# Performance work log

Measured on AMD Instinct MI355X. Metric: run time of the kernel, lower is better.

The kernel has to match this reference:

```python
import jax, jax.numpy as jnp
import numpy as np

B, S, D, H = 4, 1024, 1024, 16
DH = D // H  # 64
SCALE = 1.0 / np.sqrt(D)  # module uses 1/sqrt(d_model), not d_head


def _mh(t):
    # [B,S,D] -> [B*H,S,DH]
    b, s, _ = t.shape
    return t.reshape(b, s, H, DH).transpose(0, 2, 1, 3).reshape(b * H, s, DH)


def _shift(t):
    # pad one zero at FRONT of last dim, reinterpret (row-major) as [BH,L+1,S], drop first row
    bh, s, l = t.shape
    t = jnp.concatenate([jnp.zeros((bh, s, 1), t.dtype), t], axis=-1)
    return t.reshape(bh, l + 1, s)[:, 1:, :]


def setup_inputs() -> dict:
    key = jax.random.key(0)
    ks = jax.random.split(key, 12)
    w_sc = 1.0 / np.sqrt(D)
    return {
        "x": jax.random.normal(ks[0], (B, S, D), jnp.float32),
        "u": jax.random.normal(ks[1], (DH,), jnp.float32) * 0.02,
        "v": jax.random.normal(ks[2], (DH,), jnp.float32) * 0.02,
        "pos": jax.random.normal(ks[3], (B, S, D), jnp.float32),
        "Wq": jax.random.normal(ks[4], (D, D), jnp.float32) * w_sc,
        "bq": jnp.zeros((D,), jnp.float32),
        "Wk": jax.random.normal(ks[5], (D, D), jnp.float32) * w_sc,
        "bk": jnp.zeros((D,), jnp.float32),
        "Wv": jax.random.normal(ks[6], (D, D), jnp.float32) * w_sc,
        "bv": jnp.zeros((D,), jnp.float32),
        "Wc": jax.random.normal(ks[7], (D, D), jnp.float32) * w_sc,
        "bc": jnp.zeros((D,), jnp.float32),
    }


def reference(x, u, v, pos, Wq, bq, Wk, bk, Wv, bv, Wc, bc):
    q = _mh(x @ Wq.T + bq)      # [BH,S,DH]
    k = _mh(x @ Wk.T + bk)      # [BH,S,DH]
    w = _mh(x @ Wv.T + bv)      # [BH,S,DH]
    r = _mh(pos)                # [BH,S,DH]
    ac = jnp.einsum('bjk,bmk->bjm', q + u, k)          # content-content  [BH,S,S]
    bd = _shift(jnp.einsum('bjk,blk->bjl', q + v, r))  # content-position [BH,S,S]
    att = jax.nn.softmax((ac + bd) * SCALE, axis=-1)   # dropout is identity (eval)
    o = att @ w                                        # [BH,S,DH]
    o = o.reshape(B, H, S, DH).transpose(0, 2, 1, 3).reshape(B, S, D)
    return o @ Wc.T + bc
```

## Files before the change

kernel.cpp:

```cpp
#include <hip/hip_runtime.h>
#include <hip/hip_bf16.h>


typedef __bf16 bf16x8 __attribute__((ext_vector_type(8)));
typedef float  f32x4  __attribute__((ext_vector_type(4)));
typedef unsigned short u16x4 __attribute__((ext_vector_type(4)));

struct alignas(16) U128 { unsigned long long lo, hi; };

__device__ __forceinline__ bf16x8 ldg8(const __hip_bfloat16* p) {
    U128 u = *reinterpret_cast<const U128*>(p);
    return __builtin_bit_cast(bf16x8, u);
}

__device__ __forceinline__ __bf16 f2b(float f) {
    __hip_bfloat16 h = __float2bfloat16(f);
    return __builtin_bit_cast(__bf16, h);
}
__device__ __forceinline__ unsigned short f2bu(float f) {
    __hip_bfloat16 h = __float2bfloat16(f);
    return __builtin_bit_cast(unsigned short, h);
}
__device__ __forceinline__ float b2f(__bf16 b) {
    __hip_bfloat16 h = __builtin_bit_cast(__hip_bfloat16, b);
    return __bfloat162float(h);
}

__device__ __forceinline__ bf16x8 ldg8cvt(const float* p) {
    f32x4 a = *reinterpret_cast<const f32x4*>(p);
    f32x4 b = *reinterpret_cast<const f32x4*>(p + 4);
    bf16x8 r;
    r[0] = f2b(a[0]); r[1] = f2b(a[1]); r[2] = f2b(a[2]); r[3] = f2b(a[3]);
    r[4] = f2b(b[0]); r[5] = f2b(b[1]); r[6] = f2b(b[2]); r[7] = f2b(b[3]);
    return r;
}

#define MFMA16(a, b, c) __builtin_amdgcn_mfma_f32_16x16x32_bf16((a), (b), (c), 0, 0, 0)

__device__ __forceinline__ void gll16(const __hip_bfloat16* g, void* lds_wave_base) {
    __builtin_amdgcn_global_load_lds(
        (const __attribute__((address_space(1))) void*)g,
        (__attribute__((address_space(3))) void*)lds_wave_base,
        16, 0, 0);
}

__global__ __launch_bounds__(256) void cvt_kernel(
    const float* __restrict__ x,  const float* __restrict__ pos,
    const float* __restrict__ wq, const float* __restrict__ wk,
    const float* __restrict__ wv, const float* __restrict__ wc,
    __hip_bfloat16* __restrict__ xb, __hip_bfloat16* __restrict__ posb,
    __hip_bfloat16* __restrict__ wqkvb, __hip_bfloat16* __restrict__ wcb)
{
    const size_t base = ((size_t)blockIdx.x * 256 + threadIdx.x) * 8;
    const size_t M1 = (size_t)1 << 20;
    const float* src; __hip_bfloat16* dst; size_t o;
    if (base < 4*M1)        { src = x;   dst = xb;           o = base; }
    else if (base < 8*M1)   { src = pos; dst = posb;         o = base - 4*M1; }
    else if (base < 9*M1)   { src = wq;  dst = wqkvb;        o = base - 8*M1; }
    else if (base < 10*M1)  { src = wk;  dst = wqkvb + M1;   o = base - 9*M1; }
    else if (base < 11*M1)  { src = wv;  dst = wqkvb + 2*M1; o = base - 10*M1; }
    else                    { src = wc;  dst = wcb;          o = base - 11*M1; }
    *(bf16x8*)(dst + o) = ldg8cvt(src + o);
}

__global__ __launch_bounds__(256) void gemm_qkv(
    const __hip_bfloat16* __restrict__ A,
    const __hip_bfloat16* __restrict__ Bm,
    const float* __restrict__ bq, const float* __restrict__ bk,
    const float* __restrict__ bv, const float* __restrict__ u,
    __hip_bfloat16* __restrict__ Qu,
    __hip_bfloat16* __restrict__ Kb, __hip_bfloat16* __restrict__ Vt)
{
    __shared__ __hip_bfloat16 As[128 * 32];
    __shared__ __hip_bfloat16 Bs[128 * 32];

    const int tid  = threadIdx.x;
    const int lane = tid & 63, w = tid >> 6;
    const int quad = lane >> 4, c16 = lane & 15;
    const int wm = w >> 1, wn = w & 1;
    const int m0 = blockIdx.y * 128;
    const int n0 = blockIdx.x * 128;

    const int srow = w * 16 + (lane >> 2);
    const int scol = (lane & 3) * 8;
    const __hip_bfloat16* gA0 = A  + (size_t)(m0 + srow) * 1024 + scol;
    const __hip_bfloat16* gA1 = gA0 + (size_t)64 * 1024;
    const __hip_bfloat16* gB0 = Bm + (size_t)(n0 + srow) * 1024 + scol;
    const __hip_bfloat16* gB1 = gB0 + (size_t)64 * 1024;
    char* ldsA0 = (char*)As + (w << 10);
    char* ldsA1 = ldsA0 + 4096;
    char* ldsB0 = (char*)Bs + (w << 10);
    char* ldsB1 = ldsB0 + 4096;

    f32x4 acc[4][4] = {};

    for (int k0 = 0; k0 < 1024; k0 += 32) {
        gll16(gA0 + k0, ldsA0);
        gll16(gA1 + k0, ldsA1);
        gll16(gB0 + k0, ldsB0);
        gll16(gB1 + k0, ldsB1);
        __syncthreads();

        bf16x8 af[4], bfr[4];
        #pragma unroll
        for (int i = 0; i < 4; ++i) {
            af[i]  = *(const bf16x8*)&As[(wm * 64 + i * 16 + c16) * 32 + quad * 8];
            bfr[i] = *(const bf16x8*)&Bs[(wn * 64 + i * 16 + c16) * 32 + quad * 8];
        }
        #pragma unroll
        for (int mi = 0; mi < 4; ++mi)
            #pragma unroll
            for (int ni = 0; ni < 4; ++ni)
                acc[mi][ni] = MFMA16(af[mi], bfr[ni], acc[mi][ni]);
        __syncthreads();
    }

    #pragma unroll
    for (int mi = 0; mi < 4; ++mi) {
        #pragma unroll
        for (int ni = 0; ni < 4; ++ni) {
            const int m = m0 + wm * 64 + mi * 16 + quad * 4;
            const int n = n0 + wn * 64 + ni * 16 + c16;
            if (n < 1024) {
                const float b0 = bq[n] + u[n & 63];
                #pragma unroll
                for (int r = 0; r < 4; ++r)
                    Qu[(size_t)(m + r) * 1024 + n] =
                        __float2bfloat16(acc[mi][ni][r] + b0);
            } else if (n < 2048) {
                const int nn = n - 1024;
                const float b0 = bk[nn];
                #pragma unroll
                for (int r = 0; r < 4; ++r)
                    Kb[(size_t)(m + r) * 1024 + nn] =
                        __float2bfloat16(acc[mi][ni][r] + b0);
            } else {
                const int nn = n - 2048;
                const float b0 = bv[nn];
                const int d = nn & 63, hh = nn >> 6;
                const int bb = m >> 10, s = m & 1023;
                u16x4 pk;
                #pragma unroll
                for (int r = 0; r < 4; ++r)
                    pk[r] = f2bu(acc[mi][ni][r] + b0);
                *(u16x4*)&Vt[(((size_t)(bb * 16 + hh) * 64 + d) << 10) + s] = pk;
            }
        }
    }
}

__global__ __launch_bounds__(256) void gemm_fin64(
    const __hip_bfloat16* __restrict__ A,
    const __hip_bfloat16* __restrict__ Bm,
    float* __restrict__ dout, const float* __restrict__ bc)
{
    __shared__ __hip_bfloat16 As[64 * 32];
    __shared__ __hip_bfloat16 Bs[64 * 32];

    const int tid  = threadIdx.x;
    const int lane = tid & 63, w = tid >> 6;
    const int quad = lane >> 4, c16 = lane & 15;
    const int wm = w >> 1, wn = w & 1;
    const int m0 = blockIdx.y * 64;
    const int n0 = blockIdx.x * 64;

    const int srow = w * 16 + (lane >> 2);
    const int scol = (lane & 3) * 8;
    const __hip_bfloat16* gA = A  + (size_t)(m0 + srow) * 1024 + scol;
    const __hip_bfloat16* gB = Bm + (size_t)(n0 + srow) * 1024 + scol;
    char* ldsA = (char*)As + (w << 10);
    char* ldsB = (char*)Bs + (w << 10);

    f32x4 acc[2][2] = {};

    for (int k0 = 0; k0 < 1024; k0 += 32) {
        gll16(gA + k0, ldsA);
        gll16(gB + k0, ldsB);
        __syncthreads();

        bf16x8 af[2], bfr[2];
        #pragma unroll
        for (int i = 0; i < 2; ++i) {
            af[i]  = *(const bf16x8*)&As[(wm * 32 + i * 16 + c16) * 32 + quad * 8];
            bfr[i] = *(const bf16x8*)&Bs[(wn * 32 + i * 16 + c16) * 32 + quad * 8];
        }
        #pragma unroll
        for (int mi = 0; mi < 2; ++mi)
            #pragma unroll
            for (int ni = 0; ni < 2; ++ni)
                acc[mi][ni] = MFMA16(af[mi], bfr[ni], acc[mi][ni]);
        __syncthreads();
    }

    #pragma unroll
    for (int mi = 0; mi < 2; ++mi) {
        #pragma unroll
        for (int ni = 0; ni < 2; ++ni) {
            const int m = m0 + wm * 32 + mi * 16 + quad * 4;
            const int n = n0 + wn * 32 + ni * 16 + c16;
            const float b0 = bc[n];
            #pragma unroll
            for (int r = 0; r < 4; ++r)
                dout[(size_t)(m + r) * 1024 + n] = acc[mi][ni][r] + b0;
        }
    }
}

__device__ __forceinline__ int lidx16(int row, int c) {
    return (row << 10) + ((((c >> 3) ^ row) << 3) | (c & 7));
}

__global__ __launch_bounds__(512) void attn_kernel(
    const __hip_bfloat16* __restrict__ Qu,
    const __hip_bfloat16* __restrict__ Kb,
    const __hip_bfloat16* __restrict__ Posb,
    const __hip_bfloat16* __restrict__ Vt,
    const float* __restrict__ uvec, const float* __restrict__ vvec,
    __hip_bfloat16* __restrict__ O)
{
    __shared__ __hip_bfloat16 Ls[64 * 1024];
    __shared__ float q2s[64];
    __shared__ float Wsum[64 * 8];
    __shared__ float rs[64];

    const int tid  = threadIdx.x;
    const int lane = tid & 63, w = tid >> 6;
    const int quad = lane >> 4, c16 = lane & 15;
    const int i0 = blockIdx.y * 64;
    const int bh = blockIdx.x;
    const int b = bh >> 4, h = bh & 15;
    const size_t headoff = (size_t)h * 64;
    const size_t tokbase = (size_t)b * 1024;
    const int j2 = i0 + 64;

    if (tid < 64) {
        float val = 0.f;
        if (j2 < 1024)
            val = b2f(__builtin_bit_cast(__bf16,
                      Qu[(tokbase + j2) * 1024 + headoff + tid])) +
                  (vvec[tid] - uvec[tid]);
        q2s[tid] = val;
    }
    __syncthreads();

    if (tid < 64) {
        const int i = i0 + tid;
        if (i + 1 < 1024) Ls[lidx16(tid, i + 1)] = __float2bfloat16(0.f);
    }

    const __hip_bfloat16* qup0 =
        Qu + (tokbase + i0 + c16) * 1024 + headoff + quad * 8;

    {
        bf16x8 a[4][2];
        #pragma unroll
        for (int g = 0; g < 4; ++g) {
            a[g][0] = ldg8(qup0 + (size_t)g * 16 * 1024);
            a[g][1] = ldg8(qup0 + (size_t)g * 16 * 1024 + 32);
            #pragma unroll
            for (int j = 0; j < 8; ++j) {
                const int d = quad * 8 + j;
                a[g][0][j] = f2b(b2f(a[g][0][j]) + (vvec[d] - uvec[d]));
                a[g][1][j] = f2b(b2f(a[g][1][j]) + (vvec[d + 32] - uvec[d + 32]));
            }
        }
        for (int t = 0; t < 8; ++t) {
            const int l0 = w * 128 + t * 16;
            const __hip_bfloat16* rp =
                Posb + (tokbase + l0 + c16) * 1024 + headoff + quad * 8;
            const bf16x8 r0 = ldg8(rp);
            const bf16x8 r1 = ldg8(rp + 32);
            const int l = l0 + c16;
            #pragma unroll
            for (int g = 0; g < 4; ++g) {
                f32x4 c = (f32x4){0.f, 0.f, 0.f, 0.f};
                c = MFMA16(a[g][0], r0, c);
                c = MFMA16(a[g][1], r1, c);
                #pragma unroll
                for (int r = 0; r < 4; ++r) {
                    const int jl = g * 16 + quad * 4 + r;
                    const int j  = i0 + jl;
                    const __bf16 val = f2b(c[r]);
                    if (l >= 1023 - j) Ls[lidx16(jl, l + j - 1023)] =
                        __builtin_bit_cast(__hip_bfloat16, val);
                    if (jl >= 1 && l <= 1022 - j) Ls[lidx16(jl - 1, l + j + 1)] =
                        __builtin_bit_cast(__hip_bfloat16, val);
                }
            }
        }
    }

    if (j2 < 1024) {
        for (int c = i0 + 65 + tid; c < 1024; c += 512) {
            const int l = c - i0 - 65;
            const __hip_bfloat16* rp = Posb + (tokbase + l) * 1024 + headoff;
            float s = 0.f;
            #pragma unroll
            for (int d8 = 0; d8 < 8; ++d8) {
                const bf16x8 rv = ldg8(rp + d8 * 8);
                #pragma unroll
                for (int j = 0; j < 8; ++j)
                    s += q2s[d8 * 8 + j] * b2f(rv[j]);
            }
            Ls[lidx16(63, c)] = __float2bfloat16(s);
        }
    }
    __syncthreads();

    {
        bf16x8 au[4][2];
        #pragma unroll
        for (int g = 0; g < 4; ++g) {
            au[g][0] = ldg8(qup0 + (size_t)g * 16 * 1024);
            au[g][1] = ldg8(qup0 + (size_t)g * 16 * 1024 + 32);
        }
        const float C1 = 1.44269504f * 0.03125f;
        const float C2 = -5.77078016f;
        float sums[4][4] = {};
        for (int t = 0; t < 8; ++t) {
            const int c0 = w * 128 + t * 16;
            const __hip_bfloat16* kp =
                Kb + (tokbase + c0 + c16) * 1024 + headoff + quad * 8;
            const bf16x8 k0 = ldg8(kp);
            const bf16x8 k1 = ldg8(kp + 32);
            const int cc = c0 + c16;
            #pragma unroll
            for (int g = 0; g < 4; ++g) {
                f32x4 c = (f32x4){0.f, 0.f, 0.f, 0.f};
                c = MFMA16(au[g][0], k0, c);
                c = MFMA16(au[g][1], k1, c);
                #pragma unroll
                for (int r = 0; r < 4; ++r) {
                    const int il = g * 16 + quad * 4 + r;
                    const int idx = lidx16(il, cc);
                    const float lg = __bfloat162float(Ls[idx]) + c[r];
                    const float p = __builtin_amdgcn_exp2f(fmaf(lg, C1, C2));
                    sums[g][r] += p;
                    Ls[idx] = __float2bfloat16(p);
                }
            }
        }
        #pragma unroll
        for (int g = 0; g < 4; ++g)
            #pragma unroll
            for (int r = 0; r < 4; ++r) {
                float s = sums[g][r];
                s += __shfl_xor(s, 1);
                s += __shfl_xor(s, 2);
                s += __shfl_xor(s, 4);
                s += __shfl_xor(s, 8);
                if (c16 == 0) Wsum[(g * 16 + quad * 4 + r) * 8 + w] = s;
            }
    }
    __syncthreads();

    if (tid < 64) {
        float s = 0.f;
        #pragma unroll
        for (int k = 0; k < 8; ++k) s += Wsum[tid * 8 + k];
        rs[tid] = 1.f / s;
    }
    __syncthreads();

    {
        const int d0 = (w & 3) * 16;
        const int kh = w >> 2;
        const __hip_bfloat16* vp =
            Vt + ((size_t)bh * 64 + d0 + c16) * 1024 + quad * 8;
        f32x4 acc[4] = {};
        for (int kk = kh * 512; kk < kh * 512 + 512; kk += 32) {
            const bf16x8 vld = ldg8(vp + kk);
            #pragma unroll
            for (int g = 0; g < 4; ++g) {
                const bf16x8 p =
                    *(const bf16x8*)&Ls[lidx16(g * 16 + c16, kk + quad * 8)];
                acc[g] = MFMA16(p, vld, acc[g]);
            }
        }
        __syncthreads();
        float* Lf = (float*)Ls;
        const int sbase = (w & 3) * 1024;
        if (kh == 1) {
            #pragma unroll
            for (int g = 0; g < 4; ++g)
                #pragma unroll
                for (int r = 0; r < 4; ++r)
                    Lf[sbase + g * 256 + (quad * 4 + r) * 16 + c16] = acc[g][r];
        }
        __syncthreads();
        if (kh == 0) {
            #pragma unroll
            for (int g = 0; g < 4; ++g)
                #pragma unroll
                for (int r = 0; r < 4; ++r) {
                    const int il = g * 16 + quad * 4 + r;
                    const float val =
                        (acc[g][r] + Lf[sbase + g * 256 + (quad * 4 + r) * 16 + c16])
                        * rs[il];
                    const int i = i0 + il;
                    const int d = d0 + c16;
                    O[(tokbase + i) * 1024 + headoff + d] = __float2bfloat16(val);
                }
        }
    }
}

extern "C" void kernel_launch(void* const* d_in, const int* in_sizes, int n_in,
                              void* d_out, int out_size, void* d_ws, size_t ws_size,
                              hipStream_t stream)
{
    const float* x   = (const float*)d_in[0];
    const float* u   = (const float*)d_in[1];
    const float* v   = (const float*)d_in[2];
    const float* pos = (const float*)d_in[3];
    const float* Wq  = (const float*)d_in[4];
    const float* bq  = (const float*)d_in[5];
    const float* Wk  = (const float*)d_in[6];
    const float* bk  = (const float*)d_in[7];
    const float* Wv  = (const float*)d_in[8];
    const float* bv  = (const float*)d_in[9];
    const float* Wc  = (const float*)d_in[10];
    const float* bc  = (const float*)d_in[11];

    const size_t MB = (size_t)1 << 20;
    char* ws = (char*)d_ws;
    __hip_bfloat16* Qu    = (__hip_bfloat16*)(ws + 0 * MB);
    __hip_bfloat16* Kb    = (__hip_bfloat16*)(ws + 8 * MB);
    __hip_bfloat16* Vt    = (__hip_bfloat16*)(ws + 16 * MB);
    __hip_bfloat16* xb    = (__hip_bfloat16*)(ws + 24 * MB);
    __hip_bfloat16* O     = (__hip_bfloat16*)(ws + 24 * MB);
    __hip_bfloat16* Posb  = (__hip_bfloat16*)(ws + 32 * MB);
    __hip_bfloat16* Wqkvb = (__hip_bfloat16*)(ws + 40 * MB);
    __hip_bfloat16* Wcb   = (__hip_bfloat16*)(ws + 46 * MB);

    cvt_kernel<<<6144, 256, 0, stream>>>(x, pos, Wq, Wk, Wv, Wc,
                                         xb, Posb, Wqkvb, Wcb);

    gemm_qkv<<<dim3(24, 32), dim3(256), 0, stream>>>(
        xb, Wqkvb, bq, bk, bv, u, Qu, Kb, Vt);

    attn_kernel<<<dim3(64, 16), dim3(512), 0, stream>>>(
        Qu, Kb, Posb, Vt, u, v, O);

    gemm_fin64<<<dim3(16, 64), dim3(256), 0, stream>>>(
        O, Wcb, (float*)d_out, bc);
}
```

Measured before the change: 281.9 us.

## Halve attention query tile to 32 rows and transpose MFMA operands for vectorized LDS access

Each attention block now handles 32 query rows instead of 64. That halves the 128KB LDS score buffer to 64KB and doubles the grid, with launch bounds hinting more resident blocks per CU. The MFMA operands are swapped so each lane holds four consecutive columns of one row. This allows packed 4-element LDS reads and writes of scores and probabilities, a simpler shift index computation, and fewer cross-lane reductions. The cost is that K, V and positional data are reloaded from global memory twice as often per query row.

```diff
diff --git a/kernel.cpp b/kernel.cpp
--- a/kernel.cpp
+++ b/kernel.cpp
@@ -23,6 +23,10 @@
 }
 __device__ __forceinline__ float b2f(__bf16 b) {
     __hip_bfloat16 h = __builtin_bit_cast(__hip_bfloat16, b);
+    return __bfloat162float(h);
+}
+__device__ __forceinline__ float bu2f(unsigned short u) {
+    __hip_bfloat16 h = __builtin_bit_cast(__hip_bfloat16, u);
     return __bfloat162float(h);
 }
 
@@ -210,7 +214,7 @@
     return (row << 10) + ((((c >> 3) ^ row) << 3) | (c & 7));
 }
 
-__global__ __launch_bounds__(512) void attn_kernel(
+__global__ __launch_bounds__(512, 4) void attn_kernel(
     const __hip_bfloat16* __restrict__ Qu,
     const __hip_bfloat16* __restrict__ Kb,
     const __hip_bfloat16* __restrict__ Posb,
@@ -218,20 +222,20 @@
     const float* __restrict__ uvec, const float* __restrict__ vvec,
     __hip_bfloat16* __restrict__ O)
 {
-    __shared__ __hip_bfloat16 Ls[64 * 1024];
+    __shared__ __attribute__((aligned(16))) __hip_bfloat16 Ls[32 * 1024];
     __shared__ float q2s[64];
-    __shared__ float Wsum[64 * 8];
-    __shared__ float rs[64];
+    __shared__ float Wsum[32 * 8];
+    __shared__ float rs[32];
 
     const int tid  = threadIdx.x;
     const int lane = tid & 63, w = tid >> 6;
     const int quad = lane >> 4, c16 = lane & 15;
-    const int i0 = blockIdx.y * 64;
+    const int i0 = blockIdx.y * 32;
     const int bh = blockIdx.x;
     const int b = bh >> 4, h = bh & 15;
     const size_t headoff = (size_t)h * 64;
     const size_t tokbase = (size_t)b * 1024;
-    const int j2 = i0 + 64;
+    const int j2 = i0 + 32;
 
     if (tid < 64) {
         float val = 0.f;
@@ -243,7 +247,7 @@
     }
     __syncthreads();
 
-    if (tid < 64) {
+    if (tid < 32) {
         const int i = i0 + tid;
         if (i + 1 < 1024) Ls[lidx16(tid, i + 1)] = __float2bfloat16(0.f);
     }
@@ -252,9 +256,9 @@
         Qu + (tokbase + i0 + c16) * 1024 + headoff + quad * 8;
 
     {
-        bf16x8 a[4][2];
-        #pragma unroll
-        for (int g = 0; g < 4; ++g) {
+        bf16x8 a[2][2];
+        #pragma unroll
+        for (int g = 0; g < 2; ++g) {
             a[g][0] = ldg8(qup0 + (size_t)g * 16 * 1024);
             a[g][1] = ldg8(qup0 + (size_t)g * 16 * 1024 + 32);
             #pragma unroll
@@ -270,91 +274,92 @@
                 Posb + (tokbase + l0 + c16) * 1024 + headoff + quad * 8;
             const bf16x8 r0 = ldg8(rp);
             const bf16x8 r1 = ldg8(rp + 32);
-            const int l = l0 + c16;
-            #pragma unroll
-            for (int g = 0; g < 4; ++g) {
+            const int lq = l0 + quad * 4;
+            #pragma unroll
+            for (int g = 0; g < 2; ++g) {
                 f32x4 c = (f32x4){0.f, 0.f, 0.f, 0.f};
-                c = MFMA16(a[g][0], r0, c);
-                c = MFMA16(a[g][1], r1, c);
+                c = MFMA16(r0, a[g][0], c);
+                c = MFMA16(r1, a[g][1], c);
+                const int jl = g * 16 + c16;
+                const int base2 = lq + i0 + jl + 1;
+                const int rwm1 = jl - 1;
                 #pragma unroll
                 for (int r = 0; r < 4; ++r) {
-                    const int jl = g * 16 + quad * 4 + r;
-                    const int j  = i0 + jl;
-                    const __bf16 val = f2b(c[r]);
-                    if (l >= 1023 - j) Ls[lidx16(jl, l + j - 1023)] =
-                        __builtin_bit_cast(__hip_bfloat16, val);
-                    if (jl >= 1 && l <= 1022 - j) Ls[lidx16(jl - 1, l + j + 1)] =
-                        __builtin_bit_cast(__hip_bfloat16, val);
+                    const int t1 = base2 + r;
+                    const int cc = t1 & 1023;
+                    const int rw = rwm1 + (t1 >> 10);
+                    if (rw >= 0)
+                        Ls[lidx16(rw, cc)] = __float2bfloat16(c[r]);
                 }
             }
         }
     }
 
     if (j2 < 1024) {
-        for (int c = i0 + 65 + tid; c < 1024; c += 512) {
-            const int l = c - i0 - 65;
+        for (int c = i0 + 33 + tid; c < 1024; c += 512) {
+            const int l = c - i0 - 33;
             const __hip_bfloat16* rp = Posb + (tokbase + l) * 1024 + headoff;
             float s = 0.f;
             #pragma unroll
             for (int d8 = 0; d8 < 8; ++d8) {
                 const bf16x8 rv = ldg8(rp + d8 * 8);
                 #pragma unroll
-                for (int j = 0; j < 8; ++j)
-                    s += q2s[d8 * 8 + j] * b2f(rv[j]);
-            }
-            Ls[lidx16(63, c)] = __float2bfloat16(s);
+                for (int jj = 0; jj < 8; ++jj)
+                    s += q2s[d8 * 8 + jj] * b2f(rv[jj]);
+            }
+            Ls[lidx16(31, c)] = __float2bfloat16(s);
         }
     }
     __syncthreads();
 
     {
-        bf16x8 au[4][2];
-        #pragma unroll
-        for (int g = 0; g < 4; ++g) {
+        bf16x8 au[2][2];
+        #pragma unroll
+        for (int g = 0; g < 2; ++g) {
             au[g][0] = ldg8(qup0 + (size_t)g * 16 * 1024);
             au[g][1] = ldg8(qup0 + (size_t)g * 16 * 1024 + 32);
         }
         const float C1 = 1.44269504f * 0.03125f;
         const float C2 = -5.77078016f;
-        float sums[4][4] = {};
+        float rsum[2] = {0.f, 0.f};
         for (int t = 0; t < 8; ++t) {
             const int c0 = w * 128 + t * 16;
             const __hip_bfloat16* kp =
                 Kb + (tokbase + c0 + c16) * 1024 + headoff + quad * 8;
             const bf16x8 k0 = ldg8(kp);
             const bf16x8 k1 = ldg8(kp + 32);
-            const int cc = c0 + c16;
-            #pragma unroll
-            for (int g = 0; g < 4; ++g) {
+            const int cc0 = c0 + quad * 4;
+            #pragma unroll
+            for (int g = 0; g < 2; ++g) {
                 f32x4 c = (f32x4){0.f, 0.f, 0.f, 0.f};
-                c = MFMA16(au[g][0], k0, c);
-                c = MFMA16(au[g][1], k1, c);
+                c = MFMA16(k0, au[g][0], c);
+                c = MFMA16(k1, au[g][1], c);
+                const int jl = g * 16 + c16;
+                const int idx = lidx16(jl, cc0);
+                const u16x4 bd = *(const u16x4*)&Ls[idx];
+                u16x4 pk;
+                float s4 = 0.f;
                 #pragma unroll
                 for (int r = 0; r < 4; ++r) {
-                    const int il = g * 16 + quad * 4 + r;
-                    const int idx = lidx16(il, cc);
-                    const float lg = __bfloat162float(Ls[idx]) + c[r];
+                    const float lg = bu2f(bd[r]) + c[r];
                     const float p = __builtin_amdgcn_exp2f(fmaf(lg, C1, C2));
-                    sums[g][r] += p;
-                    Ls[idx] = __float2bfloat16(p);
+                    s4 += p;
+                    pk[r] = f2bu(p);
                 }
-            }
-        }
-        #pragma unroll
-        for (int g = 0; g < 4; ++g)
-            #pragma unroll
-            for (int r = 0; r < 4; ++r) {
-                float s = sums[g][r];
-                s += __shfl_xor(s, 1);
-                s += __shfl_xor(s, 2);
-                s += __shfl_xor(s, 4);
-                s += __shfl_xor(s, 8);
-                if (c16 == 0) Wsum[(g * 16 + quad * 4 + r) * 8 + w] = s;
-            }
+                *(u16x4*)&Ls[idx] = pk;
+                s4 += __shfl_xor(s4, 16);
+                s4 += __shfl_xor(s4, 32);
+                rsum[g] += s4;
+            }
+        }
+        if (lane < 16) {
+            Wsum[lane * 8 + w] = rsum[0];
+            Wsum[(16 + lane) * 8 + w] = rsum[1];
+        }
     }
     __syncthreads();
 
-    if (tid < 64) {
+    if (tid < 32) {
         float s = 0.f;
         #pragma unroll
         for (int k = 0; k < 8; ++k) s += Wsum[tid * 8 + k];
@@ -367,11 +372,11 @@
         const int kh = w >> 2;
         const __hip_bfloat16* vp =
             Vt + ((size_t)bh * 64 + d0 + c16) * 1024 + quad * 8;
-        f32x4 acc[4] = {};
+        f32x4 acc[2] = {};
         for (int kk = kh * 512; kk < kh * 512 + 512; kk += 32) {
             const bf16x8 vld = ldg8(vp + kk);
             #pragma unroll
-            for (int g = 0; g < 4; ++g) {
+            for (int g = 0; g < 2; ++g) {
                 const bf16x8 p =
                     *(const bf16x8*)&Ls[lidx16(g * 16 + c16, kk + quad * 8)];
                 acc[g] = MFMA16(p, vld, acc[g]);
@@ -382,7 +387,7 @@
         const int sbase = (w & 3) * 1024;
         if (kh == 1) {
             #pragma unroll
-            for (int g = 0; g < 4; ++g)
+            for (int g = 0; g < 2; ++g)
                 #pragma unroll
                 for (int r = 0; r < 4; ++r)
                     Lf[sbase + g * 256 + (quad * 4 + r) * 16 + c16] = acc[g][r];
@@ -390,7 +395,7 @@
         __syncthreads();
         if (kh == 0) {
             #pragma unroll
-            for (int g = 0; g < 4; ++g)
+            for (int g = 0; g < 2; ++g)
                 #pragma unroll
                 for (int r = 0; r < 4; ++r) {
                     const int il = g * 16 + quad * 4 + r;
@@ -439,7 +444,7 @@
     gemm_qkv<<<dim3(24, 32), dim3(256), 0, stream>>>(
         xb, Wqkvb, bq, bk, bv, u, Qu, Kb, Vt);
 
-    attn_kernel<<<dim3(64, 16), dim3(512), 0, stream>>>(
+    attn_kernel<<<dim3(64, 32), dim3(512), 0, stream>>>(
         Qu, Kb, Posb, Vt, u, v, O);
 
     gemm_fin64<<<dim3(16, 64), dim3(256), 0, stream>>>(
```

Result: slower. 289.6 us (+2.7%).
